# Kernel optimization log

Measured on AMD Instinct MI355X. Metric: run time of the kernel, lower is better.

## Reference

```python
import jax, jax.numpy as jnp
import numpy as np

DIM = 1024
H = 16
D = DIM // H
SCALE = D ** -0.5
EPS = 1e-5


def _layernorm(x, w, b):
    # force_fp32 LayerNorm over last axis
    xf = x.astype(jnp.float32)
    mu = xf.mean(-1, keepdims=True)
    var = xf.var(-1, keepdims=True)
    y = (xf - mu) / jnp.sqrt(var + EPS) * w.astype(jnp.float32) + b.astype(jnp.float32)
    return y.astype(x.dtype)


def setup_inputs() -> dict:
    key = jax.random.key(0)
    ks = jax.random.split(key, 8)
    x = jax.random.normal(ks[0], (2, 2048, DIM), dtype=jnp.float32)
    qkv_w = jax.random.normal(ks[1], (3 * DIM, DIM), dtype=jnp.float32) * (DIM ** -0.5)
    q_norm_w = jnp.ones((D,), jnp.float32)
    q_norm_b = jnp.zeros((D,), jnp.float32)
    k_norm_w = jnp.ones((D,), jnp.float32)
    k_norm_b = jnp.zeros((D,), jnp.float32)
    proj_w = jax.random.normal(ks[2], (DIM, DIM), dtype=jnp.float32) * (DIM ** -0.5)
    proj_b = jnp.zeros((DIM,), jnp.float32)
    return {"x": x, "qkv_w": qkv_w, "q_norm_w": q_norm_w, "q_norm_b": q_norm_b,
            "k_norm_w": k_norm_w, "k_norm_b": k_norm_b, "proj_w": proj_w, "proj_b": proj_b}


def reference(x, qkv_w, q_norm_w, q_norm_b, k_norm_w, k_norm_b, proj_w, proj_b):
    B, N, C = x.shape
    qkv = x @ qkv_w.T                                  # [B,N,3C]
    qkv = qkv.reshape(B, N, 3, H, D).transpose(2, 0, 3, 1, 4)  # [3,B,H,N,D]
    q, k, v = qkv[0], qkv[1], qkv[2]
    # per-head QK LayerNorm over head_dim
    q = _layernorm(q, q_norm_w, q_norm_b)
    k = _layernorm(k, k_norm_w, k_norm_b)
    # k-centering across sequence
    k = k - k.mean(-2, keepdims=True)
    attn = jnp.einsum('bhnd,bhmd->bhnm', q * SCALE, k)
    attn = attn - attn.max(-1, keepdims=True)
    attn = jax.nn.softmax(attn, axis=-1)
    out = jnp.einsum('bhnm,bhmd->bhnd', attn, v)       # [B,H,N,D]
    out = out.transpose(0, 2, 1, 3).reshape(B, N, C)
    return out @ proj_w.T + proj_b
```

## Files before the change

kernel.cpp:

```cpp
#include <hip/hip_runtime.h>
#include <cstdint>
#include <cstddef>

#define SEQ     2048
#define NBATCH  2
#define CDIM    1024
#define NHEAD   16
#define HDIM    64
#define MTOT    (NBATCH*SEQ)
#define C3      (3*CDIM)
#define LOG2E   1.44269504088896340736f
#define QKSCALE (0.125f*LOG2E)
#define LN_EPS  1e-5f

typedef unsigned short u16;
typedef short s16x8 __attribute__((ext_vector_type(8)));
typedef float f32x4  __attribute__((ext_vector_type(4)));
typedef float f32x16 __attribute__((ext_vector_type(16)));

static __device__ __forceinline__ f32x4 mfma16(s16x8 a, s16x8 b, f32x4 c) {
  return __builtin_amdgcn_mfma_f32_16x16x32_bf16(a, b, c, 0, 0, 0);
}
static __device__ __forceinline__ f32x16 mfma32(s16x8 a, s16x8 b, f32x16 c) {
  return __builtin_amdgcn_mfma_f32_32x32x16_bf16(a, b, c, 0, 0, 0);
}
static __device__ __forceinline__ float b2f(u16 v) {
  return __uint_as_float(((unsigned)v) << 16);
}
static __device__ __forceinline__ u16 f2b(float f) {
  unsigned u = __float_as_uint(f);
  u = u + 0x7fffu + ((u >> 16) & 1u);
  return (u16)(u >> 16);
}
static __device__ __forceinline__ float fexp2(float x) {
  float r;
  asm("v_exp_f32 %0, %1" : "=v"(r) : "v"(x));
  return r;
}

#define G2L16(g, l) __builtin_amdgcn_global_load_lds( \
    (__attribute__((address_space(1))) void*)(g),     \
    (__attribute__((address_space(3))) void*)(l), 16, 0, 0)

#define XSEG   (MTOT*CDIM/8)
#define W1SEG  (C3*CDIM/8)
#define W2SEG  (CDIM*CDIM/8)
__global__ __launch_bounds__(256) void cast_all(
    const float* __restrict__ x, const float* __restrict__ w1,
    const float* __restrict__ w2, u16* __restrict__ xb,
    u16* __restrict__ wqkv, u16* __restrict__ wproj)
{
  int i = blockIdx.x * 256 + threadIdx.x;
  const float* src; u16* dst; int off;
  if (i < XSEG)              { src = x;  dst = xb;    off = i; }
  else if (i < XSEG + W1SEG) { src = w1; dst = wqkv;  off = i - XSEG; }
  else                       { src = w2; dst = wproj; off = i - XSEG - W1SEG; }
  float4 a = ((const float4*)src)[2*off];
  float4 b = ((const float4*)src)[2*off+1];
  union { u16 u[8]; uint4 v; } r;
  r.u[0]=f2b(a.x); r.u[1]=f2b(a.y); r.u[2]=f2b(a.z); r.u[3]=f2b(a.w);
  r.u[4]=f2b(b.x); r.u[5]=f2b(b.y); r.u[6]=f2b(b.z); r.u[7]=f2b(b.w);
  ((uint4*)dst)[off] = r.v;
}

template<bool WRITE_BF16, bool BIAS>
__global__ __launch_bounds__(256) void gemm_nt(
    const u16* __restrict__ A, const u16* __restrict__ Bm,
    void* __restrict__ Cout, const float* __restrict__ bias,
    int M, int Nn, int K)
{
  __shared__ u16 As[128*64];
  __shared__ u16 Bs[128*64];
  const int tid = threadIdx.x;
  const int wave = tid >> 6, lane = tid & 63;
  const int l15 = lane & 15, l4 = lane >> 4;
  const int m0 = blockIdx.x * 128, n0 = blockIdx.y * 128;
  const int wr = (wave >> 1) * 64, wc = (wave & 1) * 64;
  f32x4 acc[4][4] = {};

  for (int k0 = 0; k0 < K; k0 += 64) {
    if (k0) __syncthreads();
#pragma unroll
    for (int i = 0; i < 4; ++i) {
      int ci  = (i*4 + wave)*64 + lane;
      int row = ci >> 3, ch = ci & 7;
      int chs = ch ^ (row & 7);
      const u16* ga = A  + (size_t)(m0 + row)*K + k0 + chs*8;
      const u16* gb = Bm + (size_t)(n0 + row)*K + k0 + chs*8;
      G2L16(ga, As + (i*4 + wave)*512);
      G2L16(gb, Bs + (i*4 + wave)*512);
    }
    __syncthreads();

#pragma unroll
    for (int kk = 0; kk < 2; ++kk) {
      s16x8 af[4], bf[4];
#pragma unroll
      for (int r = 0; r < 4; ++r) {
        int row = wr + r*16 + l15;
        af[r] = *(const s16x8*)(As + row*64 + (((kk*4 + l4) ^ (row & 7))*8));
      }
#pragma unroll
      for (int c = 0; c < 4; ++c) {
        int row = wc + c*16 + l15;
        bf[c] = *(const s16x8*)(Bs + row*64 + (((kk*4 + l4) ^ (row & 7))*8));
      }
#pragma unroll
      for (int r = 0; r < 4; ++r)
#pragma unroll
        for (int c = 0; c < 4; ++c)
          acc[r][c] = mfma16(af[r], bf[c], acc[r][c]);
    }
  }

#pragma unroll
  for (int r = 0; r < 4; ++r)
#pragma unroll
    for (int c = 0; c < 4; ++c) {
      int row = m0 + wr + r*16 + l4*4;
      int col = n0 + wc + c*16 + l15;
#pragma unroll
      for (int q = 0; q < 4; ++q) {
        float v = acc[r][c][q];
        if (BIAS) v += bias[col];
        if (WRITE_BF16) ((u16*)Cout)[(size_t)(row + q)*Nn + col] = f2b(v);
        else           ((float*)Cout)[(size_t)(row + q)*Nn + col] = v;
      }
    }
}

__global__ __launch_bounds__(256) void ln_qk(
    const u16* __restrict__ qkv,
    const float* __restrict__ qw, const float* __restrict__ qb,
    const float* __restrict__ kw, const float* __restrict__ kb,
    u16* __restrict__ Qs, u16* __restrict__ Kn)
{
  const int tid = threadIdx.x, wave = tid >> 6, lane = tid & 63;
  const int m = blockIdx.x*2 + (wave >> 1);
  const int part = wave & 1;
  const int b = m >> 11, n = m & 2047;
  const float* wv = part ? kw : qw;
  const float* bv = part ? kb : qb;
  u16* dst = part ? Kn : Qs;
  const float scale = part ? 1.f : QKSCALE;
  const u16* base = qkv + (size_t)m*C3 + part*CDIM;
  const int d0 = (lane & 7) * 8;
  float wl[8], bl[8];
#pragma unroll
  for (int j = 0; j < 8; ++j) { wl[j] = wv[d0+j]*scale; bl[j] = bv[d0+j]*scale; }
#pragma unroll
  for (int c = 0; c < 2; ++c) {
    int h = c*8 + (lane >> 3);
    s16x8 v = *(const s16x8*)(base + c*512 + lane*8);
    float f[8]; float s = 0.f, s2 = 0.f;
#pragma unroll
    for (int j = 0; j < 8; ++j) {
      f[j] = b2f((u16)v[j]); s += f[j]; s2 += f[j]*f[j];
    }
#pragma unroll
    for (int off = 1; off < 8; off <<= 1) {
      s += __shfl_xor(s, off, 64); s2 += __shfl_xor(s2, off, 64);
    }
    float mu = s*(1.f/64.f);
    float rs = rsqrtf(s2*(1.f/64.f) - mu*mu + LN_EPS);
    union { u16 u[8]; uint4 q; } r;
#pragma unroll
    for (int j = 0; j < 8; ++j)
      r.u[j] = f2b((f[j]-mu)*rs*wl[j] + bl[j]);
    *(uint4*)(dst + ((size_t)(b*NHEAD+h)*SEQ + n)*HDIM + d0) = r.q;
  }
}

__global__ __launch_bounds__(256) void v_transpose(
    const u16* __restrict__ qkv, u16* __restrict__ Vt)
{
  __shared__ u16 t[64][80];
  int bh = blockIdx.x, j0 = blockIdx.y * 64;
  int b = bh >> 4, h = bh & 15;
  int tid = threadIdx.x;
  int nl = tid >> 2, ch = tid & 3;
  const u16* src = qkv + (size_t)(b*SEQ + j0 + nl)*C3 + 2*CDIM + h*HDIM + ch*16;
  *(uint4*)&t[nl][ch*16]     = *(const uint4*)src;
  *(uint4*)&t[nl][ch*16 + 8] = *(const uint4*)(src + 8);
  __syncthreads();
  int d = tid >> 2, nc = tid & 3;
  u16 o[16];
#pragma unroll
  for (int i = 0; i < 16; ++i) o[i] = t[nc*16 + i][d];
  u16* dst = Vt + ((size_t)(bh*HDIM + d))*SEQ + j0 + nc*16;
  *(uint4*)dst       = *(uint4*)&o[0];
  *(uint4*)(dst + 8) = *(uint4*)&o[8];
}

__global__ __launch_bounds__(256) void flash_attn(
    const u16* __restrict__ Qs, const u16* __restrict__ Kn,
    const u16* __restrict__ Vt, u16* __restrict__ Oa)
{
  __shared__ u16 Kt[2][64*64];
  __shared__ u16 Vs[2][64*64];
  const int tid = threadIdx.x, wave = tid >> 6, lane = tid & 63;
  const int l31 = lane & 31, hi = lane >> 5;
  const int bid0 = blockIdx.x + blockIdx.y*16;
  const int nid  = (bid0 & 7)*64 + (bid0 >> 3);
  const int bh   = nid >> 4;
  const int q0   = (nid & 15)*128 + wave*32;
  const int sw = l31 & 7;

  const u16* Qrow = Qs + ((size_t)bh*SEQ + q0 + l31)*HDIM + hi*8;
  s16x8 qf[4];
#pragma unroll
  for (int ks = 0; ks < 4; ++ks)
    qf[ks] = *(const s16x8*)(Qrow + ks*16);

  f32x16 o0 = {}, o1 = {};
  float l_run = 0.f;

  const u16* Kg = Kn + (size_t)bh*SEQ*HDIM;
  const u16* Vg = Vt + (size_t)bh*HDIM*SEQ;

  auto STAGE = [&](int jb, int buf) {
#pragma unroll
    for (int i = 0; i < 2; ++i) {
      int ci = (i*4 + wave)*64 + lane;
      int row = ci >> 3, ch = ci & 7;
      int chs = ch ^ (row & 7);
      G2L16(Kg + (size_t)(jb + row)*HDIM + chs*8, Kt[buf] + (i*4 + wave)*512);
      G2L16(Vg + (size_t)row*SEQ + jb + chs*8,    Vs[buf] + (i*4 + wave)*512);
    }
  };

  STAGE(0, 0);
  __syncthreads();

  const int NT = SEQ/64;
  for (int t = 0; t < NT; ++t) {
    const int buf = t & 1;
    if (t + 1 < NT) STAGE((t+1)*64, buf ^ 1);
    const u16* Kb = Kt[buf];
    const u16* Vb = Vs[buf];

    f32x16 s0 = {}, s1 = {};
    __builtin_amdgcn_s_setprio(1);
#pragma unroll
    for (int ks = 0; ks < 4; ++ks) {
      int ch = ((ks*2 + hi) ^ sw) * 8;
      s16x8 k0 = *(const s16x8*)(Kb + l31*64 + ch);
      s16x8 k1 = *(const s16x8*)(Kb + (32 + l31)*64 + ch);
      s0 = mfma32(k0, qf[ks], s0);
      s1 = mfma32(k1, qf[ks], s1);
    }
    __builtin_amdgcn_s_setprio(0);

    float p0[16], p1[16];
#pragma unroll
    for (int i = 0; i < 16; ++i) p0[i] = fexp2(s0[i]);
#pragma unroll
    for (int i = 0; i < 16; ++i) p1[i] = fexp2(s1[i]);
    float s8[8];
#pragma unroll
    for (int i = 0; i < 8; ++i) s8[i] = (p0[i] + p0[i+8]) + (p1[i] + p1[i+8]);
    l_run += ((s8[0]+s8[1]) + (s8[2]+s8[3])) + ((s8[4]+s8[5]) + (s8[6]+s8[7]));

    s16x8 pf[4];
#pragma unroll
    for (int f = 0; f < 2; ++f) {
      const float* pp = f ? p1 : p0;
      unsigned pk[4][2];
#pragma unroll
      for (int q = 0; q < 4; ++q)
#pragma unroll
        for (int i = 0; i < 2; ++i)
          asm("v_cvt_pk_bf16_f32 %0, %1, %2"
              : "=v"(pk[q][i]) : "v"(pp[4*q+2*i]), "v"(pp[4*q+2*i+1]));
#pragma unroll
      for (int kc = 0; kc < 2; ++kc) {
        union { unsigned u[4]; s16x8 v; } bfu;
#pragma unroll
        for (int i = 0; i < 2; ++i) {
          unsigned x = pk[2*kc][i], y = pk[2*kc+1][i];
          asm("v_permlane32_swap_b32 %0, %1" : "+v"(x), "+v"(y));
          bfu.u[i] = x; bfu.u[2+i] = y;
        }
        pf[2*f+kc] = bfu.v;
      }
    }

    __builtin_amdgcn_s_setprio(1);
#pragma unroll
    for (int s = 0; s < 4; ++s) {
      int ch = ((s*2 + hi) ^ sw) * 8;
      s16x8 v0 = *(const s16x8*)(Vb + l31*64 + ch);
      s16x8 v1 = *(const s16x8*)(Vb + (32 + l31)*64 + ch);
      o0 = mfma32(v0, pf[s], o0);
      o1 = mfma32(v1, pf[s], o1);
    }
    __builtin_amdgcn_s_setprio(0);
    __syncthreads();
  }

  float l_all = l_run + __shfl_xor(l_run, 32, 64);
  float inv = 1.f / l_all;
  int b = bh >> 4, h = bh & 15;
  u16* dst = Oa + ((size_t)(b*SEQ + q0 + l31))*CDIM + h*HDIM;
#pragma unroll
  for (int df = 0; df < 2; ++df)
#pragma unroll
    for (int q2 = 0; q2 < 4; ++q2) {
      float a0, a1, a2, a3;
      if (df) { a0=o1[4*q2]; a1=o1[4*q2+1]; a2=o1[4*q2+2]; a3=o1[4*q2+3]; }
      else    { a0=o0[4*q2]; a1=o0[4*q2+1]; a2=o0[4*q2+2]; a3=o0[4*q2+3]; }
      a0 *= inv; a1 *= inv; a2 *= inv; a3 *= inv;
      unsigned w0, w1;
      asm("v_cvt_pk_bf16_f32 %0, %1, %2" : "=v"(w0) : "v"(a0), "v"(a1));
      asm("v_cvt_pk_bf16_f32 %0, %1, %2" : "=v"(w1) : "v"(a2), "v"(a3));
      uint2 st; st.x = w0; st.y = w1;
      *(uint2*)(dst + df*32 + q2*8 + hi*4) = st;
    }
}

extern "C" void kernel_launch(void* const* d_in, const int* in_sizes, int n_in,
                              void* d_out, int out_size, void* d_ws, size_t ws_size,
                              hipStream_t stream)
{
  const float* x      = (const float*)d_in[0];
  const float* qkv_w  = (const float*)d_in[1];
  const float* qnw    = (const float*)d_in[2];
  const float* qnb    = (const float*)d_in[3];
  const float* knw    = (const float*)d_in[4];
  const float* knb    = (const float*)d_in[5];
  const float* proj_w = (const float*)d_in[6];
  const float* proj_b = (const float*)d_in[7];
  float* out = (float*)d_out;

  char* ws = (char*)d_ws;
  u16* xb    = (u16*)(ws);
  u16* wqkv  = (u16*)(ws + (8ull  << 20));
  u16* wproj = (u16*)(ws + (14ull << 20));
  u16* qkvb  = (u16*)(ws + (16ull << 20));
  u16* Qsb   = (u16*)(ws + (40ull << 20));
  u16* Knb   = (u16*)(ws + (48ull << 20));
  u16* Vtb   = (u16*)(ws + (56ull << 20));
  u16* Oab   = (u16*)(ws + (64ull << 20));

  cast_all<<<(XSEG + W1SEG + W2SEG)/256, 256, 0, stream>>>(
      x, qkv_w, proj_w, xb, wqkv, wproj);

  gemm_nt<true, false><<<dim3(MTOT/128, C3/128), 256, 0, stream>>>(
      xb, wqkv, qkvb, nullptr, MTOT, C3, CDIM);

  ln_qk<<<MTOT/2, 256, 0, stream>>>(qkvb, qnw, qnb, knw, knb, Qsb, Knb);
  v_transpose<<<dim3(NBATCH*NHEAD, SEQ/64), 256, 0, stream>>>(qkvb, Vtb);

  flash_attn<<<dim3(SEQ/128, NBATCH*NHEAD), 256, 0, stream>>>(Qsb, Knb, Vtb, Oab);

  gemm_nt<false, true><<<dim3(MTOT/128, CDIM/128), 256, 0, stream>>>(
      Oab, wproj, out, proj_b, MTOT, CDIM, CDIM);
}
```

Baseline: 198.5 us.

## Software-pipeline flash attention: overlap next QK and softmax with current PV, triple-buffer

Restructures the flash-attention inner loop so that QK^T for tile t+1 is issued before PV for tile t, and the exp/convert for t+1 runs after that PV. This lets MFMA work overlap the transcendental and permute work. K/V shared-memory staging moves from double to triple buffering, prefetching two tiles ahead. The cost is more LDS per block (48KB vs 32KB) and more live registers for the extra score and P fragments, which may lower occupancy.

```diff
diff --git a/kernel.cpp b/kernel.cpp
--- a/kernel.cpp
+++ b/kernel.cpp
@@ -196,8 +196,8 @@
     const u16* __restrict__ Qs, const u16* __restrict__ Kn,
     const u16* __restrict__ Vt, u16* __restrict__ Oa)
 {
-  __shared__ u16 Kt[2][64*64];
-  __shared__ u16 Vs[2][64*64];
+  __shared__ u16 Kt[3][64*64];
+  __shared__ u16 Vs[3][64*64];
   const int tid = threadIdx.x, wave = tid >> 6, lane = tid & 63;
   const int l31 = lane & 31, hi = lane >> 5;
   const int bid0 = blockIdx.x + blockIdx.y*16;
@@ -229,17 +229,7 @@
     }
   };
 
-  STAGE(0, 0);
-  __syncthreads();
-
-  const int NT = SEQ/64;
-  for (int t = 0; t < NT; ++t) {
-    const int buf = t & 1;
-    if (t + 1 < NT) STAGE((t+1)*64, buf ^ 1);
-    const u16* Kb = Kt[buf];
-    const u16* Vb = Vs[buf];
-
-    f32x16 s0 = {}, s1 = {};
+  auto QK = [&](const u16* Kb, f32x16& s0, f32x16& s1) {
     __builtin_amdgcn_s_setprio(1);
 #pragma unroll
     for (int ks = 0; ks < 4; ++ks) {
@@ -250,7 +240,9 @@
       s1 = mfma32(k1, qf[ks], s1);
     }
     __builtin_amdgcn_s_setprio(0);
-
+  };
+
+  auto SM = [&](const f32x16& s0, const f32x16& s1, s16x8* pf) {
     float p0[16], p1[16];
 #pragma unroll
     for (int i = 0; i < 16; ++i) p0[i] = fexp2(s0[i]);
@@ -260,8 +252,6 @@
 #pragma unroll
     for (int i = 0; i < 8; ++i) s8[i] = (p0[i] + p0[i+8]) + (p1[i] + p1[i+8]);
     l_run += ((s8[0]+s8[1]) + (s8[2]+s8[3])) + ((s8[4]+s8[5]) + (s8[6]+s8[7]));
-
-    s16x8 pf[4];
 #pragma unroll
     for (int f = 0; f < 2; ++f) {
       const float* pp = f ? p1 : p0;
@@ -284,7 +274,9 @@
         pf[2*f+kc] = bfu.v;
       }
     }
-
+  };
+
+  auto PV = [&](const u16* Vb, const s16x8* pf) {
     __builtin_amdgcn_s_setprio(1);
 #pragma unroll
     for (int s = 0; s < 4; ++s) {
@@ -295,8 +287,33 @@
       o1 = mfma32(v1, pf[s], o1);
     }
     __builtin_amdgcn_s_setprio(0);
+  };
+
+  const int NT = SEQ/64;
+  STAGE(0, 0);
+  __syncthreads();
+  STAGE(64, 1);
+  s16x8 pfC[4];
+  {
+    f32x16 s0 = {}, s1 = {};
+    QK(Kt[0], s0, s1);
+    SM(s0, s1, pfC);
+  }
+  __syncthreads();
+  STAGE(128, 2);
+
+  for (int t = 0; t < NT-1; ++t) {
+    f32x16 n0 = {}, n1 = {};
+    QK(Kt[(t+1)%3], n0, n1);
+    s16x8 pfN[4];
+    PV(Vs[t%3], pfC);
+    SM(n0, n1, pfN);
     __syncthreads();
+    if (t + 3 < NT) STAGE((t+3)*64, (t+3)%3);
+#pragma unroll
+    for (int i = 0; i < 4; ++i) pfC[i] = pfN[i];
   }
+  PV(Vs[(NT-1)%3], pfC);
 
   float l_all = l_run + __shfl_xor(l_run, 32, 64);
   float inv = 1.f / l_all;
```

New measurement: 192.8 us. -2.9%, faster.
